# Kernel tuning notes

Measured on AMD Instinct MI355X. Metric: run time of the kernel, lower is better.

## Reference

```python
import jax, jax.numpy as jnp
import numpy as np

H = 32

def setup_inputs() -> dict:
    key = jax.random.key(0)
    ks = jax.random.split(key, 8)
    B, S = 256, 4096
    scale = 1.0 / np.sqrt(H)
    return {
        "lstm_outputs": jax.random.normal(ks[0], (B, S, H), dtype=jnp.float32),
        "final_hidden": jax.random.normal(ks[1], (B, H), dtype=jnp.float32),
        "Wq": jax.random.uniform(ks[2], (H, H), jnp.float32, -scale, scale),
        "bq": jax.random.uniform(ks[3], (H,), jnp.float32, -scale, scale),
        "Wk": jax.random.uniform(ks[4], (H, H), jnp.float32, -scale, scale),
        "bk": jax.random.uniform(ks[5], (H,), jnp.float32, -scale, scale),
        "Wv": jax.random.uniform(ks[6], (H, 1), jnp.float32, -scale, scale),
        "bv": jax.random.uniform(ks[7], (1,), jnp.float32, -scale, scale),
    }

def reference(lstm_outputs, final_hidden, Wq, bq, Wk, bk, Wv, bv):
    # keys: [B,S,H], query: [B,H]
    keys = jnp.einsum('bsh,hd->bsd', lstm_outputs, Wk) + bk
    query = final_hidden @ Wq + bq
    tanhed = jnp.tanh(query[:, None, :] + keys)            # [B,S,H]
    scores = jnp.einsum('bsh,h->bs', tanhed, Wv[:, 0]) + bv[0]  # [B,S]
    att_weights = jax.nn.softmax(scores, axis=-1)          # [B,S]
    context = jnp.einsum('bs,bsh->bh', att_weights, keys)  # [B,H]
    return context, att_weights
```

## Files before the change

kernel.cpp:

```cpp
#include <hip/hip_runtime.h>
#include <math.h>

#define HD 32
#define BB 256
#define SS 4096
#define BLK 256
#define POSB 256
#define NCH (SS / POSB)
#define PADW 40
#define PSTRIDE 33

typedef short bf16x8 __attribute__((ext_vector_type(8)));
typedef float f32x4 __attribute__((ext_vector_type(4)));

__device__ __forceinline__ float tanh_fast(float x) {
  float e = __builtin_amdgcn_exp2f(x * 2.8853900817779268f);
  return 1.0f - 2.0f * __builtin_amdgcn_rcpf(e + 1.0f);
}
__device__ __forceinline__ float exp_fast(float x) {
  return __builtin_amdgcn_exp2f(x * 1.4426950408889634f);
}
__device__ __forceinline__ short bf16_trunc(float x) {
  return (short)(__float_as_uint(x) >> 16);
}
__device__ __forceinline__ float hi_part(float x) {
  return __uint_as_float(__float_as_uint(x) & 0xffff0000u);
}

__global__ void __launch_bounds__(BLK, 4) bahdanau_p1(
    const float* __restrict__ lstm, const float* __restrict__ fh,
    const float* __restrict__ Wq, const float* __restrict__ bq,
    const float* __restrict__ Wk, const float* __restrict__ bk,
    const float* __restrict__ Wv, const float* __restrict__ bv,
    float* __restrict__ scores_out, float* __restrict__ partials) {
  __shared__ short sWkTh[HD * PADW];
  __shared__ short sWkTl[HD * PADW];
  __shared__ float sQB[HD];
  __shared__ float sWv[HD];
  __shared__ float sYp[4][HD];
  __shared__ float sRedL[4];

  const int tid = threadIdx.x;
  const int b = blockIdx.x >> 4;
  const int chunk = blockIdx.x & (NCH - 1);
  const int base = chunk * POSB;
  const int lane = tid & 63, w = tid >> 6;
  const int col = lane & 15, quad = lane >> 4;

  {
    float4 w4 = ((const float4*)Wk)[tid];
    const int k = tid >> 3, h0 = (tid & 7) * 4;
    const float v[4] = {w4.x, w4.y, w4.z, w4.w};
#pragma unroll
    for (int i = 0; i < 4; i++) {
      const float hf = hi_part(v[i]);
      sWkTh[(h0 + i) * PADW + k] = bf16_trunc(v[i]);
      sWkTl[(h0 + i) * PADW + k] = bf16_trunc(v[i] - hf);
    }
  }
  if (tid < HD) {
    float acc = bq[tid] + bk[tid];
    const float* fhb = fh + b * HD;
#pragma unroll
    for (int j = 0; j < HD; j++) acc += fhb[j] * Wq[j * HD + tid];
    sQB[tid] = acc;
    sWv[tid] = Wv[tid];
  }
  __syncthreads();

  bf16x8 Bh0 = *(const bf16x8*)&sWkTh[(col) * PADW + quad * 8];
  bf16x8 Bl0 = *(const bf16x8*)&sWkTl[(col) * PADW + quad * 8];
  bf16x8 Bh1 = *(const bf16x8*)&sWkTh[(16 + col) * PADW + quad * 8];
  bf16x8 Bl1 = *(const bf16x8*)&sWkTl[(16 + col) * PADW + quad * 8];
  const float qb0 = sQB[col], qb1 = sQB[16 + col];
  const float wv0 = sWv[col], wv1 = sWv[16 + col];
  const float bv0 = bv[0];

  const float* gx = lstm + ((size_t)b * SS + base + w * 64) * HD;
  float lAcc = 0.f;
  float yp[8];
#pragma unroll
  for (int j = 0; j < 8; j++) yp[j] = 0.f;

#pragma unroll
  for (int mt = 0; mt < 4; mt++) {
    const float* rp = gx + (size_t)(mt * 16 + col) * HD + quad * 8;
    const float4 xa = ((const float4*)rp)[0];
    const float4 xb = ((const float4*)rp)[1];
    const float xs[8] = {xa.x, xa.y, xa.z, xa.w, xb.x, xb.y, xb.z, xb.w};
    bf16x8 Ah, Al;
#pragma unroll
    for (int j = 0; j < 8; j++) {
      const float hf = hi_part(xs[j]);
      Ah[j] = bf16_trunc(xs[j]);
      Al[j] = bf16_trunc(xs[j] - hf);
    }
    f32x4 c0 = {0.f, 0.f, 0.f, 0.f}, c1 = {0.f, 0.f, 0.f, 0.f};
    c0 = __builtin_amdgcn_mfma_f32_16x16x32_bf16(Ah, Bh0, c0, 0, 0, 0);
    c0 = __builtin_amdgcn_mfma_f32_16x16x32_bf16(Al, Bh0, c0, 0, 0, 0);
    c0 = __builtin_amdgcn_mfma_f32_16x16x32_bf16(Ah, Bl0, c0, 0, 0, 0);
    c1 = __builtin_amdgcn_mfma_f32_16x16x32_bf16(Ah, Bh1, c1, 0, 0, 0);
    c1 = __builtin_amdgcn_mfma_f32_16x16x32_bf16(Al, Bh1, c1, 0, 0, 0);
    c1 = __builtin_amdgcn_mfma_f32_16x16x32_bf16(Ah, Bl1, c1, 0, 0, 0);

    float esc[4];
#pragma unroll
    for (int r = 0; r < 4; r++) {
      float t = tanh_fast(qb0 + c0[r]) * wv0 + tanh_fast(qb1 + c1[r]) * wv1;
      t += __shfl_xor(t, 1, 64);
      t += __shfl_xor(t, 2, 64);
      t += __shfl_xor(t, 4, 64);
      t += __shfl_xor(t, 8, 64);
      esc[r] = exp_fast(t + bv0);
    }
    const int srcLane = (col >> 2) * 16;
    const float g0 = __shfl(esc[0], srcLane, 64);
    const float g1 = __shfl(esc[1], srcLane, 64);
    const float g2 = __shfl(esc[2], srcLane, 64);
    const float g3 = __shfl(esc[3], srcLane, 64);
    const int rr = col & 3;
    const float e_m = (rr == 0) ? g0 : (rr == 1) ? g1 : (rr == 2) ? g2 : g3;
    if (lane < 16)
      scores_out[(size_t)b * SS + base + w * 64 + mt * 16 + lane] = e_m;
    lAcc += (lane < 16) ? e_m : 0.f;
#pragma unroll
    for (int j = 0; j < 8; j++) yp[j] = fmaf(e_m, xs[j], yp[j]);
  }

#pragma unroll
  for (int j = 0; j < 8; j++) {
    yp[j] += __shfl_xor(yp[j], 1, 64);
    yp[j] += __shfl_xor(yp[j], 2, 64);
    yp[j] += __shfl_xor(yp[j], 4, 64);
    yp[j] += __shfl_xor(yp[j], 8, 64);
  }
  if (col == 0) {
#pragma unroll
    for (int j = 0; j < 8; j++) sYp[w][quad * 8 + j] = yp[j];
  }
#pragma unroll
  for (int off = 32; off >= 1; off >>= 1) lAcc += __shfl_xor(lAcc, off, 64);
  if (lane == 0) sRedL[w] = lAcc;
  __syncthreads();

  if (tid < HD) {
    float y = sYp[0][tid] + sYp[1][tid] + sYp[2][tid] + sYp[3][tid];
    float* p = partials + (size_t)blockIdx.x * PSTRIDE;
    p[1 + tid] = y;
    if (tid == 0) p[0] = sRedL[0] + sRedL[1] + sRedL[2] + sRedL[3];
  }
}

__global__ void __launch_bounds__(BLK) bahdanau_p2(
    const float* __restrict__ partials, const float* __restrict__ Wk,
    const float* __restrict__ bk, float* __restrict__ ctx_out,
    float* __restrict__ scores) {
  const int blk = blockIdx.x;
  const int b = blk >> 2;
  const int tid = threadIdx.x;
  __shared__ float sY[HD];

  float L = 0.f;
#pragma unroll
  for (int c = 0; c < NCH; c++)
    L += partials[(size_t)(b * NCH + c) * PSTRIDE];
  const float invL = __builtin_amdgcn_rcpf(L);

  if ((blk & 3) == 0) {
    if (tid < HD) {
      float y = 0.f;
#pragma unroll
      for (int c = 0; c < NCH; c++)
        y += partials[(size_t)(b * NCH + c) * PSTRIDE + 1 + tid];
      sY[tid] = y;
    }
    __syncthreads();
    if (tid < HD) {
      float c = bk[tid] * L;
#pragma unroll
      for (int j = 0; j < HD; j++) c = fmaf(sY[j], Wk[j * HD + tid], c);
      ctx_out[b * HD + tid] = c * invL;
    }
  }

  float4* srow = (float4*)(scores + (size_t)b * SS + (blk & 3) * 1024);
  float4 s = srow[tid];
  s.x *= invL; s.y *= invL; s.z *= invL; s.w *= invL;
  srow[tid] = s;
}

extern "C" void kernel_launch(void* const* d_in, const int* in_sizes, int n_in,
                              void* d_out, int out_size, void* d_ws,
                              size_t ws_size, hipStream_t stream) {
  const float* lstm = (const float*)d_in[0];
  const float* fh   = (const float*)d_in[1];
  const float* Wq   = (const float*)d_in[2];
  const float* bq   = (const float*)d_in[3];
  const float* Wk   = (const float*)d_in[4];
  const float* bk   = (const float*)d_in[5];
  const float* Wv   = (const float*)d_in[6];
  const float* bv   = (const float*)d_in[7];

  float* out = (float*)d_out;
  float* ctx_out = out;
  float* scores = out + BB * HD;
  float* partials = (float*)d_ws;

  bahdanau_p1<<<BB * NCH, BLK, 0, stream>>>(lstm, fh, Wq, bq, Wk, bk, Wv, bv,
                                            scores, partials);
  bahdanau_p2<<<BB * 4, BLK, 0, stream>>>(partials, Wk, bk, ctx_out, scores);
}
```

Measured before the change: 212.0 us.

## Hoist query/Wk split into prep kernel; give each wave 256 rows with register prefetch

Adds a small prep kernel that computes the per-batch query vectors and the hi/lo bf16 split of Wk once, in MFMA operand order. The main kernel then has no LDS setup or block barrier, and each wave independently handles 256 positions. It double-buffers global loads of the next 64 rows in registers while computing the current ones. Partials are written per wave with float4 stores. This removes redundant per-block setup and hides load latency, at the cost of an extra launch, higher register pressure (launch bound lowered to 3) and fewer blocks.

```diff
diff --git a/kernel.cpp b/kernel.cpp
--- a/kernel.cpp
+++ b/kernel.cpp
@@ -5,10 +5,8 @@
 #define BB 256
 #define SS 4096
 #define BLK 256
-#define POSB 256
-#define NCH (SS / POSB)
-#define PADW 40
-#define PSTRIDE 33
+#define NCH 16
+#define PSTRIDE 36
 
 typedef short bf16x8 __attribute__((ext_vector_type(8)));
 typedef float f32x4 __attribute__((ext_vector_type(4)));
@@ -27,104 +25,131 @@
   return __uint_as_float(__float_as_uint(x) & 0xffff0000u);
 }
 
-__global__ void __launch_bounds__(BLK, 4) bahdanau_p1(
-    const float* __restrict__ lstm, const float* __restrict__ fh,
-    const float* __restrict__ Wq, const float* __restrict__ bq,
-    const float* __restrict__ Wk, const float* __restrict__ bk,
-    const float* __restrict__ Wv, const float* __restrict__ bv,
-    float* __restrict__ scores_out, float* __restrict__ partials) {
-  __shared__ short sWkTh[HD * PADW];
-  __shared__ short sWkTl[HD * PADW];
-  __shared__ float sQB[HD];
-  __shared__ float sWv[HD];
-  __shared__ float sYp[4][HD];
-  __shared__ float sRedL[4];
-
-  const int tid = threadIdx.x;
-  const int b = blockIdx.x >> 4;
-  const int chunk = blockIdx.x & (NCH - 1);
-  const int base = chunk * POSB;
-  const int lane = tid & 63, w = tid >> 6;
-  const int col = lane & 15, quad = lane >> 4;
-
-  {
-    float4 w4 = ((const float4*)Wk)[tid];
-    const int k = tid >> 3, h0 = (tid & 7) * 4;
-    const float v[4] = {w4.x, w4.y, w4.z, w4.w};
-#pragma unroll
-    for (int i = 0; i < 4; i++) {
-      const float hf = hi_part(v[i]);
-      sWkTh[(h0 + i) * PADW + k] = bf16_trunc(v[i]);
-      sWkTl[(h0 + i) * PADW + k] = bf16_trunc(v[i] - hf);
-    }
-  }
+
+__global__ void __launch_bounds__(64) bahdanau_p0(
+    const float* __restrict__ fh, const float* __restrict__ Wq,
+    const float* __restrict__ bq, const float* __restrict__ Wk,
+    const float* __restrict__ bk, float* __restrict__ qvec,
+    short* __restrict__ wkt) {
+  const int b = blockIdx.x, tid = threadIdx.x;
   if (tid < HD) {
     float acc = bq[tid] + bk[tid];
     const float* fhb = fh + b * HD;
 #pragma unroll
     for (int j = 0; j < HD; j++) acc += fhb[j] * Wq[j * HD + tid];
-    sQB[tid] = acc;
-    sWv[tid] = Wv[tid];
-  }
-  __syncthreads();
-
-  bf16x8 Bh0 = *(const bf16x8*)&sWkTh[(col) * PADW + quad * 8];
-  bf16x8 Bl0 = *(const bf16x8*)&sWkTl[(col) * PADW + quad * 8];
-  bf16x8 Bh1 = *(const bf16x8*)&sWkTh[(16 + col) * PADW + quad * 8];
-  bf16x8 Bl1 = *(const bf16x8*)&sWkTl[(16 + col) * PADW + quad * 8];
-  const float qb0 = sQB[col], qb1 = sQB[16 + col];
-  const float wv0 = sWv[col], wv1 = sWv[16 + col];
+    qvec[b * HD + tid] = acc;
+  }
+  if (b == 0) {
+    const int col = tid & 15, quad = tid >> 4;
+#pragma unroll
+    for (int j = 0; j < 8; j++) {
+      const int k = quad * 8 + j;
+      const float w0 = Wk[k * HD + col];
+      const float w1 = Wk[k * HD + 16 + col];
+      wkt[(0 * 64 + tid) * 8 + j] = bf16_trunc(w0);
+      wkt[(1 * 64 + tid) * 8 + j] = bf16_trunc(w0 - hi_part(w0));
+      wkt[(2 * 64 + tid) * 8 + j] = bf16_trunc(w1);
+      wkt[(3 * 64 + tid) * 8 + j] = bf16_trunc(w1 - hi_part(w1));
+    }
+  }
+}
+
+__global__ void __launch_bounds__(BLK, 3) bahdanau_p1(
+    const float* __restrict__ lstm, const float* __restrict__ qvec,
+    const short* __restrict__ wkt, const float* __restrict__ Wv,
+    const float* __restrict__ bv, float* __restrict__ scores_out,
+    float* __restrict__ partials) {
+  const int tid = threadIdx.x;
+  const int lane = tid & 63;
+  const int g = blockIdx.x * 4 + (tid >> 6);
+  const int b = g >> 4;
+  const int qtr = g & 15;
+  const int base = qtr * 256;
+  const int col = lane & 15, quad = lane >> 4;
+
+  const bf16x8 Bh0 = *(const bf16x8*)&wkt[(0 * 64 + lane) * 8];
+  const bf16x8 Bl0 = *(const bf16x8*)&wkt[(1 * 64 + lane) * 8];
+  const bf16x8 Bh1 = *(const bf16x8*)&wkt[(2 * 64 + lane) * 8];
+  const bf16x8 Bl1 = *(const bf16x8*)&wkt[(3 * 64 + lane) * 8];
+  const float qb0 = qvec[b * HD + col];
+  const float qb1 = qvec[b * HD + 16 + col];
+  const float wv0 = Wv[col], wv1 = Wv[16 + col];
   const float bv0 = bv[0];
 
-  const float* gx = lstm + ((size_t)b * SS + base + w * 64) * HD;
+  const float* gx = lstm + ((size_t)b * SS + base) * HD;
+  const float* rp = gx + (size_t)col * HD + quad * 8;
+
   float lAcc = 0.f;
   float yp[8];
 #pragma unroll
   for (int j = 0; j < 8; j++) yp[j] = 0.f;
 
+  float4 cur[8];
 #pragma unroll
   for (int mt = 0; mt < 4; mt++) {
-    const float* rp = gx + (size_t)(mt * 16 + col) * HD + quad * 8;
-    const float4 xa = ((const float4*)rp)[0];
-    const float4 xb = ((const float4*)rp)[1];
-    const float xs[8] = {xa.x, xa.y, xa.z, xa.w, xb.x, xb.y, xb.z, xb.w};
-    bf16x8 Ah, Al;
-#pragma unroll
-    for (int j = 0; j < 8; j++) {
-      const float hf = hi_part(xs[j]);
-      Ah[j] = bf16_trunc(xs[j]);
-      Al[j] = bf16_trunc(xs[j] - hf);
-    }
-    f32x4 c0 = {0.f, 0.f, 0.f, 0.f}, c1 = {0.f, 0.f, 0.f, 0.f};
-    c0 = __builtin_amdgcn_mfma_f32_16x16x32_bf16(Ah, Bh0, c0, 0, 0, 0);
-    c0 = __builtin_amdgcn_mfma_f32_16x16x32_bf16(Al, Bh0, c0, 0, 0, 0);
-    c0 = __builtin_amdgcn_mfma_f32_16x16x32_bf16(Ah, Bl0, c0, 0, 0, 0);
-    c1 = __builtin_amdgcn_mfma_f32_16x16x32_bf16(Ah, Bh1, c1, 0, 0, 0);
-    c1 = __builtin_amdgcn_mfma_f32_16x16x32_bf16(Al, Bh1, c1, 0, 0, 0);
-    c1 = __builtin_amdgcn_mfma_f32_16x16x32_bf16(Ah, Bl1, c1, 0, 0, 0);
-
-    float esc[4];
-#pragma unroll
-    for (int r = 0; r < 4; r++) {
-      float t = tanh_fast(qb0 + c0[r]) * wv0 + tanh_fast(qb1 + c1[r]) * wv1;
-      t += __shfl_xor(t, 1, 64);
-      t += __shfl_xor(t, 2, 64);
-      t += __shfl_xor(t, 4, 64);
-      t += __shfl_xor(t, 8, 64);
-      esc[r] = exp_fast(t + bv0);
-    }
-    const int srcLane = (col >> 2) * 16;
-    const float g0 = __shfl(esc[0], srcLane, 64);
-    const float g1 = __shfl(esc[1], srcLane, 64);
-    const float g2 = __shfl(esc[2], srcLane, 64);
-    const float g3 = __shfl(esc[3], srcLane, 64);
-    const int rr = col & 3;
-    const float e_m = (rr == 0) ? g0 : (rr == 1) ? g1 : (rr == 2) ? g2 : g3;
-    if (lane < 16)
-      scores_out[(size_t)b * SS + base + w * 64 + mt * 16 + lane] = e_m;
-    lAcc += (lane < 16) ? e_m : 0.f;
-#pragma unroll
-    for (int j = 0; j < 8; j++) yp[j] = fmaf(e_m, xs[j], yp[j]);
+    cur[2 * mt + 0] = ((const float4*)(rp + (size_t)mt * 16 * HD))[0];
+    cur[2 * mt + 1] = ((const float4*)(rp + (size_t)mt * 16 * HD))[1];
+  }
+
+#pragma unroll
+  for (int s = 0; s < 4; s++) {
+    float4 nxt[8];
+    if (s < 3) {
+      const float* rn = rp + (size_t)(s + 1) * 64 * HD;
+#pragma unroll
+      for (int mt = 0; mt < 4; mt++) {
+        nxt[2 * mt + 0] = ((const float4*)(rn + (size_t)mt * 16 * HD))[0];
+        nxt[2 * mt + 1] = ((const float4*)(rn + (size_t)mt * 16 * HD))[1];
+      }
+    }
+
+#pragma unroll
+    for (int mt = 0; mt < 4; mt++) {
+      const float4 XA = cur[2 * mt + 0], XB = cur[2 * mt + 1];
+      const float xs[8] = {XA.x, XA.y, XA.z, XA.w, XB.x, XB.y, XB.z, XB.w};
+      bf16x8 Ah, Al;
+#pragma unroll
+      for (int j = 0; j < 8; j++) {
+        const float hf = hi_part(xs[j]);
+        Ah[j] = bf16_trunc(xs[j]);
+        Al[j] = bf16_trunc(xs[j] - hf);
+      }
+      f32x4 c0 = {0.f, 0.f, 0.f, 0.f}, c1 = {0.f, 0.f, 0.f, 0.f};
+      c0 = __builtin_amdgcn_mfma_f32_16x16x32_bf16(Ah, Bh0, c0, 0, 0, 0);
+      c1 = __builtin_amdgcn_mfma_f32_16x16x32_bf16(Ah, Bh1, c1, 0, 0, 0);
+      c0 = __builtin_amdgcn_mfma_f32_16x16x32_bf16(Al, Bh0, c0, 0, 0, 0);
+      c1 = __builtin_amdgcn_mfma_f32_16x16x32_bf16(Al, Bh1, c1, 0, 0, 0);
+      c0 = __builtin_amdgcn_mfma_f32_16x16x32_bf16(Ah, Bl0, c0, 0, 0, 0);
+      c1 = __builtin_amdgcn_mfma_f32_16x16x32_bf16(Ah, Bl1, c1, 0, 0, 0);
+
+      float esc[4];
+#pragma unroll
+      for (int r = 0; r < 4; r++) {
+        float t = tanh_fast(qb0 + c0[r]) * wv0 + tanh_fast(qb1 + c1[r]) * wv1;
+        t += __shfl_xor(t, 1, 64);
+        t += __shfl_xor(t, 2, 64);
+        t += __shfl_xor(t, 4, 64);
+        t += __shfl_xor(t, 8, 64);
+        esc[r] = exp_fast(t + bv0);
+      }
+      const int srcLane = (col >> 2) * 16;
+      const float g0 = __shfl(esc[0], srcLane, 64);
+      const float g1 = __shfl(esc[1], srcLane, 64);
+      const float g2 = __shfl(esc[2], srcLane, 64);
+      const float g3 = __shfl(esc[3], srcLane, 64);
+      const int rr = col & 3;
+      const float e_m = (rr == 0) ? g0 : (rr == 1) ? g1 : (rr == 2) ? g2 : g3;
+      if (lane < 16)
+        scores_out[(size_t)b * SS + base + s * 64 + mt * 16 + lane] = e_m;
+      lAcc += (lane < 16) ? e_m : 0.f;
+#pragma unroll
+      for (int j = 0; j < 8; j++) yp[j] = fmaf(e_m, xs[j], yp[j]);
+    }
+
+    if (s < 3) {
+#pragma unroll
+      for (int i = 0; i < 8; i++) cur[i] = nxt[i];
+    }
   }
 
 #pragma unroll
@@ -134,20 +159,16 @@
     yp[j] += __shfl_xor(yp[j], 4, 64);
     yp[j] += __shfl_xor(yp[j], 8, 64);
   }
+#pragma unroll
+  for (int off = 32; off >= 1; off >>= 1) lAcc += __shfl_xor(lAcc, off, 64);
+
+  float* p = partials + (size_t)g * PSTRIDE;
+  if (lane == 0) p[0] = lAcc;
   if (col == 0) {
-#pragma unroll
-    for (int j = 0; j < 8; j++) sYp[w][quad * 8 + j] = yp[j];
-  }
-#pragma unroll
-  for (int off = 32; off >= 1; off >>= 1) lAcc += __shfl_xor(lAcc, off, 64);
-  if (lane == 0) sRedL[w] = lAcc;
-  __syncthreads();
-
-  if (tid < HD) {
-    float y = sYp[0][tid] + sYp[1][tid] + sYp[2][tid] + sYp[3][tid];
-    float* p = partials + (size_t)blockIdx.x * PSTRIDE;
-    p[1 + tid] = y;
-    if (tid == 0) p[0] = sRedL[0] + sRedL[1] + sRedL[2] + sRedL[3];
+    float4 y0 = {yp[0], yp[1], yp[2], yp[3]};
+    float4 y1 = {yp[4], yp[5], yp[6], yp[7]};
+    *(float4*)(p + 4 + quad * 8) = y0;
+    *(float4*)(p + 8 + quad * 8) = y1;
   }
 }
 
@@ -171,7 +192,7 @@
       float y = 0.f;
 #pragma unroll
       for (int c = 0; c < NCH; c++)
-        y += partials[(size_t)(b * NCH + c) * PSTRIDE + 1 + tid];
+        y += partials[(size_t)(b * NCH + c) * PSTRIDE + 4 + tid];
       sY[tid] = y;
     }
     __syncthreads();
@@ -204,9 +225,14 @@
   float* out = (float*)d_out;
   float* ctx_out = out;
   float* scores = out + BB * HD;
-  float* partials = (float*)d_ws;
-
-  bahdanau_p1<<<BB * NCH, BLK, 0, stream>>>(lstm, fh, Wq, bq, Wk, bk, Wv, bv,
-                                            scores, partials);
+
+  char* ws = (char*)d_ws;
+  float* qvec = (float*)ws;
+  short* wkt = (short*)(ws + 32768);
+  float* partials = (float*)(ws + 65536);
+
+  bahdanau_p0<<<BB, 64, 0, stream>>>(fh, Wq, bq, Wk, bk, qvec, wkt);
+  bahdanau_p1<<<BB * NCH / 4, BLK, 0, stream>>>(lstm, qvec, wkt, Wv, bv,
+                                                scores, partials);
   bahdanau_p2<<<BB * 4, BLK, 0, stream>>>(partials, Wk, bk, ctx_out, scores);
 }
```

Result: slower. 237.7 us (+12.2%).
